# Optimization experiments

Hardware: AMD Instinct MI355X
Metric: run time of the kernel (lower is better)

Reference implementation:

```python
import jax, jax.numpy as jnp
import numpy as np

BINS = 70
HLO, HHI = -10.0, 10.0
EPS = 1e-5


def _conv_bn(x, w, b, g, be, relu=True):
    # 1x1 Conv1d == channel matmul: x [B,C,N], w [O,C]
    y = jnp.einsum('oc,bcn->bon', w, x) + b[None, :, None]
    # BatchNorm1d in training mode: biased batch stats over (batch, points)
    m = jnp.mean(y, axis=(0, 2))
    v = jnp.var(y, axis=(0, 2))
    y = (y - m[None, :, None]) * jax.lax.rsqrt(v + EPS)[None, :, None]
    y = y * g[None, :, None] + be[None, :, None]
    return jax.nn.relu(y) if relu else y


def _batch_hist(x):
    # Faithful to the torch.histc global-offset hack: one flat histogram with
    # bins*B*F buckets and group offsets of exactly (HHI-HLO); values that fall
    # outside [HLO,HHI] for a given (b,f) leak into neighboring groups, exactly
    # as in the original. Returns argmax bin index per (b,f) as float.
    B, F, N = x.shape
    w = (HHI - HLO) / BINS  # 2/7, and group offset 20 == BINS*w so bins align
    total = BINS * B * F
    grp = jnp.arange(B * F, dtype=jnp.int32).reshape(B, F, 1)
    gidx = jnp.floor((x - HLO) / w).astype(jnp.int32) + BINS * grp
    gidx = jnp.where((gidx >= 0) & (gidx < total), gidx, total)  # drop out-of-range
    counts = jnp.zeros(total + 1, jnp.float32).at[gidx.ravel()].add(1.0)
    h = counts[:total].reshape(B, F, BINS)
    return jnp.argmax(h, axis=-1).astype(jnp.float32)  # [B,F]


def setup_inputs() -> dict:
    key = jax.random.key(0)
    ks = jax.random.split(key, 7)
    d = {
        'x': jax.random.normal(ks[0], (16, 3, 4096), dtype=jnp.float32),
        'w1': jax.random.normal(ks[1], (64, 3), dtype=jnp.float32) * 0.2,
        'b1': jnp.zeros((64,), jnp.float32),
        'g1': jnp.ones((64,), jnp.float32),
        'be1': jnp.zeros((64,), jnp.float32),
        'w2': jax.random.normal(ks[2], (128, 64), dtype=jnp.float32) * 0.1,
        'b2': jnp.zeros((128,), jnp.float32),
        'g2': jnp.ones((128,), jnp.float32),
        'be2': jnp.zeros((128,), jnp.float32),
        'w3': jax.random.normal(ks[3], (1024, 128), dtype=jnp.float32) * 0.08,
        'b3': jnp.zeros((1024,), jnp.float32),
        'g3': jnp.ones((1024,), jnp.float32),
        'be3': jnp.zeros((1024,), jnp.float32),
    }
    return d


def reference(x, w1, b1, g1, be1, w2, b2, g2, be2, w3, b3, g3, be3):
    # PointNetEncoder forward, global_feat=True, robust_type='HS',
    # input/feature transforms disabled (trans, trans_feat are None).
    h = _conv_bn(x, w1, b1, g1, be1, relu=True)    # [B,64,N]
    h = _conv_bn(h, w2, b2, g2, be2, relu=True)    # [B,128,N]
    h = _conv_bn(h, w3, b3, g3, be3, relu=False)   # [B,1024,N]
    feat = _batch_hist(h)                          # [B,1024] mode-bin indices
    return feat
```

## Files before the change

### kernel.cpp

```cpp
#include <hip/hip_runtime.h>

#define EPSF 1e-5f
#define TOTBINS 1146880

typedef _Float16 v8h __attribute__((ext_vector_type(8)));
typedef _Float16 v4h __attribute__((ext_vector_type(4)));
typedef float v4f __attribute__((ext_vector_type(4)));

#define OFF_PARTX   1146880
#define OFF_W1F     1149952
#define OFF_B1F     1150144
#define OFF_PMU1    1150208
#define OFF_M1N     1166592
#define OFF_MU1     1170688
#define OFF_W2H     1170752
#define OFF_W2L     1174848
#define OFF_B2F     1178944
#define OFF_PMU2    1179072
#define OFF_M2N     1211840
#define OFF_MU2     1228224
#define OFF_W3H     1228352
#define OFF_W3L     1293888
#define OFF_B3F     1359424
#define OFF_H1H     1360448
#define OFF_H1L     3457600
#define OFF_H2H     5554752
#define OFF_H2L     9749056

#define GLL(src,dst) __builtin_amdgcn_global_load_lds( \
    (const __attribute__((address_space(1))) void*)(src), \
    (__attribute__((address_space(3))) void*)(dst), 16, 0, 0)

__global__ void k_statsX(const float* __restrict__ x, float* __restrict__ part){
  __shared__ float red[12][256];
  int t = threadIdx.x;
  int s = blockIdx.x*256 + t;
  int b = s >> 12, n = s & 4095;
  const float* xb = x + (size_t)b*12288 + n;
  float x0 = xb[0], x1 = xb[4096], x2 = xb[8192];
  float v[12] = {x0,x1,x2, x0*x0,x0*x1,x0*x2, x1*x1,x1*x2,x2*x2, 0.f,0.f,0.f};
  #pragma unroll
  for(int j=0;j<12;j++) red[j][t]=v[j];
  __syncthreads();
  for(int off=128; off>0; off>>=1){
    if(t<off){
      #pragma unroll
      for(int j=0;j<12;j++) red[j][t]+=red[j][t+off];
    }
    __syncthreads();
  }
  if(t<12) part[blockIdx.x*12+t]=red[t][0];
}

__global__ void k_fold1(const float* __restrict__ part,
                        const float* __restrict__ w1, const float* __restrict__ b1,
                        const float* __restrict__ g1, const float* __restrict__ be1,
                        float* __restrict__ W1f, float* __restrict__ B1f){
  __shared__ double S[12];
  int t=threadIdx.x;
  if(t<12){
    double a=0.0;
    for(int s=0;s<256;s++) a+=(double)part[s*12+t];
    S[t]=a;
  }
  __syncthreads();
  if(t<64){
    double inv = 1.0/65536.0;
    double mu[3]={S[0]*inv,S[1]*inv,S[2]*inv};
    double M[3][3];
    M[0][0]=S[3]*inv; M[0][1]=S[4]*inv; M[0][2]=S[5]*inv;
    M[1][1]=S[6]*inv; M[1][2]=S[7]*inv; M[2][2]=S[8]*inv;
    M[1][0]=M[0][1]; M[2][0]=M[0][2]; M[2][1]=M[1][2];
    double w[3]={(double)w1[t*3],(double)w1[t*3+1],(double)w1[t*3+2]};
    double wm=0.0, q=0.0;
    for(int c=0;c<3;c++){
      wm += w[c]*mu[c];
      for(int d=0;d<3;d++) q += w[c]*w[d]*M[c][d];
    }
    double var = q - wm*wm;
    double m = wm + (double)b1[t];
    double sc = (double)g1[t] / sqrt(var + (double)EPSF);
    for(int c=0;c<3;c++) W1f[t*3+c]=(float)(w[c]*sc);
    B1f[t]=(float)(((double)b1[t]-m)*sc + (double)be1[t]);
  }
}

__global__ void k_l1s1(const float* __restrict__ x, const float* __restrict__ W1f,
                       const float* __restrict__ B1f,
                       _Float16* __restrict__ h1h, _Float16* __restrict__ h1l,
                       float* __restrict__ partM, float* __restrict__ partMu){
  __shared__ __align__(16) float tl[64][68];
  __shared__ float Wls[192];
  __shared__ float Bls[64];
  int t=threadIdx.x, wg=blockIdx.x;
  int s0=wg*256;
  int b=s0>>12, n0=s0&4095;
  int ti=t&15, tj=t>>4;
  if(t<192) Wls[t]=W1f[t];
  if(t<64)  Bls[t]=B1f[t];
  float acc[4][4];
  #pragma unroll
  for(int i=0;i<4;i++){
    #pragma unroll
    for(int j=0;j<4;j++) acc[i][j]=0.f;
  }
  float mu=0.f;
  for(int tile=0; tile<4; tile++){
    int nb=n0+tile*64;
    __syncthreads();
    {
      int nr=t>>2, cq=(t&3)<<4;
      int n=nb+nr;
      const float* xb = x + (size_t)b*12288 + n;
      float x0=xb[0], x1=xb[4096], x2=xb[8192];
      size_t off = ((size_t)((b<<12)+n))<<6;
      #pragma unroll
      for(int q=0;q<2;q++){
        v8h vh, vl;
        float4 r0, r1;
        #pragma unroll
        for(int e=0;e<8;e++){
          int f=cq+q*8+e;
          float v = fmaf(Wls[f*3+2],x2, fmaf(Wls[f*3+1],x1, fmaf(Wls[f*3],x0, Bls[f])));
          v = v>0.f ? v : 0.f;
          _Float16 hh=(_Float16)v;
          _Float16 ll=(_Float16)(v-(float)hh);
          vh[e]=hh; vl[e]=ll;
          float rec=(float)hh+(float)ll;
          if(e<4) ((float*)&r0)[e]=rec; else ((float*)&r1)[e-4]=rec;
        }
        *(v8h*)(h1h+off+cq+q*8)=vh;
        *(v8h*)(h1l+off+cq+q*8)=vl;
        *(float4*)&tl[nr][cq+q*8]   = r0;
        *(float4*)&tl[nr][cq+q*8+4] = r1;
      }
    }
    __syncthreads();
    for(int k=0;k<64;k++){
      float4 av = *(const float4*)&tl[k][ti*4];
      float4 bv = *(const float4*)&tl[k][tj*4];
      float a[4]={av.x,av.y,av.z,av.w};
      float bb[4]={bv.x,bv.y,bv.z,bv.w};
      #pragma unroll
      for(int i=0;i<4;i++){
        #pragma unroll
        for(int j=0;j<4;j++) acc[i][j]=fmaf(a[i],bb[j],acc[i][j]);
      }
    }
    if(t<64){
      float ss=0.f;
      for(int k=0;k<64;k++) ss+=tl[k][t];
      mu+=ss;
    }
  }
  #pragma unroll
  for(int i=0;i<4;i++){
    #pragma unroll
    for(int j=0;j<4;j++)
      partM[(size_t)wg*4096+(ti*4+i)*64+(tj*4+j)]=acc[i][j];
  }
  if(t<64) partMu[wg*64+t]=mu;
}

__global__ void k_reduceM1(const float* __restrict__ partM, const float* __restrict__ partMu,
                           float* __restrict__ M1n, float* __restrict__ mu1){
  int e=blockIdx.x*256+threadIdx.x;
  double a=0.0;
  for(int s=0;s<256;s++) a+=(double)partM[(size_t)s*4096+e];
  M1n[e]=(float)(a/65536.0);
  if(e<64){
    double m=0.0;
    for(int s=0;s<256;s++) m+=(double)partMu[s*64+e];
    mu1[e]=(float)(m/65536.0);
  }
}

__global__ void k_fold2(const float* __restrict__ w2, const float* __restrict__ b2,
                        const float* __restrict__ g2, const float* __restrict__ be2,
                        const float* __restrict__ M1n, const float* __restrict__ mu1,
                        _Float16* __restrict__ w2h, _Float16* __restrict__ w2l,
                        float* __restrict__ B2f){
  int f=blockIdx.x, t=threadIdx.x;
  __shared__ float w[64];
  w[t]=w2[f*64+t];
  __syncthreads();
  double tm=0.0;
  for(int c=0;c<64;c++) tm += (double)w[c]*(double)M1n[c*64+t];
  double pv=tm*(double)w[t];
  double pm=(double)w[t]*(double)mu1[t];
  #pragma unroll
  for(int off=32;off>0;off>>=1){
    pv+=__shfl_xor(pv,off,64);
    pm+=__shfl_xor(pm,off,64);
  }
  double var=pv-pm*pm;
  double m=pm+(double)b2[f];
  double sc=(double)g2[f]/sqrt(var+(double)EPSF);
  float Wf=(float)((double)w[t]*sc);
  _Float16 hh=(_Float16)Wf;
  w2h[f*64+t]=hh;
  w2l[f*64+t]=(_Float16)(Wf-(float)hh);
  if(t==0) B2f[f]=(float)(((double)b2[f]-m)*sc+(double)be2[f]);
}

__global__ __launch_bounds__(256,4) void k_layer2(
    const _Float16* __restrict__ h1h, const _Float16* __restrict__ h1l,
    const _Float16* __restrict__ w2h, const _Float16* __restrict__ w2l,
    const float* __restrict__ B2f,
    _Float16* __restrict__ h2h, _Float16* __restrict__ h2l){
  __shared__ __align__(16) _Float16 stage[4][512];
  int t=threadIdx.x, wg=blockIdx.x;
  int wv=t>>6, l=t&63;
  int lrow=l&15, lgrp=l>>4;
  int b=wg>>6;
  int n0=(wg&63)<<6;
  v8h Ah[2][2], Al[2][2];
  #pragma unroll
  for(int T=0;T<2;T++){
    const _Float16* ph = w2h + (size_t)(wv*32 + T*16 + lrow)*64 + lgrp*8;
    const _Float16* pl = w2l + (size_t)(wv*32 + T*16 + lrow)*64 + lgrp*8;
    #pragma unroll
    for(int s=0;s<2;s++){
      Ah[T][s]=*(const v8h*)(ph+s*32);
      Al[T][s]=*(const v8h*)(pl+s*32);
    }
  }
  float bias[2][4];
  #pragma unroll
  for(int T=0;T<2;T++){
    #pragma unroll
    for(int rr=0;rr<4;rr++) bias[T][rr]=B2f[wv*32+T*16+lgrp*4+rr];
  }
  int ks=wv>>1, pln=wv&1;
  const _Float16* src = (pln ? h1l : h1h)
      + (((size_t)((b<<12)+n0+lrow))<<6) + ks*32 + lgrp*8;
  _Float16* dst = &stage[wv][0];
  for(int it=0; it<4; it++){
    GLL(src,dst);
    src += 1024;
    __syncthreads();
    v8h Bh[2],Bl[2];
    #pragma unroll
    for(int s=0;s<2;s++){
      Bh[s]=*(const v8h*)&stage[s*2  ][l*8];
      Bl[s]=*(const v8h*)&stage[s*2+1][l*8];
    }
    int n=n0+it*16+lrow;
    #pragma unroll
    for(int T=0;T<2;T++){
      v4f acc={bias[T][0],bias[T][1],bias[T][2],bias[T][3]};
      #pragma unroll
      for(int s=0;s<2;s++){
        acc=__builtin_amdgcn_mfma_f32_16x16x32_f16(Ah[T][s],Bh[s],acc,0,0,0);
        acc=__builtin_amdgcn_mfma_f32_16x16x32_f16(Ah[T][s],Bl[s],acc,0,0,0);
        acc=__builtin_amdgcn_mfma_f32_16x16x32_f16(Al[T][s],Bh[s],acc,0,0,0);
      }
      size_t o=(((size_t)((b<<12)+n))<<7) + wv*32 + T*16 + lgrp*4;
      v4h sh, sl4;
      #pragma unroll
      for(int rr=0;rr<4;rr++){
        float v=acc[rr];
        v = v>0.f ? v : 0.f;
        _Float16 hh=(_Float16)v;
        sh[rr]=hh;
        sl4[rr]=(_Float16)(v-(float)hh);
      }
      *(v4h*)(h2h+o)=sh;
      *(v4h*)(h2l+o)=sl4;
    }
    __syncthreads();
  }
}

__global__ void k_stats2(const _Float16* __restrict__ h2h, const _Float16* __restrict__ h2l,
                         float* __restrict__ partM, float* __restrict__ partMu){
  __shared__ __align__(16) float tl[64][132];
  int t=threadIdx.x, wg=blockIdx.x;
  int s0=wg*256;
  int b=s0>>12, n0=s0&4095;
  int ti=t&15, tj=t>>4;
  float acc[8][8];
  #pragma unroll
  for(int i=0;i<8;i++){
    #pragma unroll
    for(int j=0;j<8;j++) acc[i][j]=0.f;
  }
  float mu=0.f;
  for(int tile=0; tile<4; tile++){
    int nb=n0+tile*64;
    __syncthreads();
    {
      int nr=t>>2, cq=(t&3)<<5;
      const _Float16* ph = h2h + ((size_t)((b<<12)+nb+nr))*128 + cq;
      const _Float16* pl = h2l + ((size_t)((b<<12)+nb+nr))*128 + cq;
      #pragma unroll
      for(int q=0;q<4;q++){
        v8h hh=*(const v8h*)(ph+q*8);
        v8h ll=*(const v8h*)(pl+q*8);
        float4 v0=make_float4((float)hh[0]+(float)ll[0],(float)hh[1]+(float)ll[1],
                              (float)hh[2]+(float)ll[2],(float)hh[3]+(float)ll[3]);
        float4 v1=make_float4((float)hh[4]+(float)ll[4],(float)hh[5]+(float)ll[5],
                              (float)hh[6]+(float)ll[6],(float)hh[7]+(float)ll[7]);
        *(float4*)&tl[nr][cq+q*8]   = v0;
        *(float4*)&tl[nr][cq+q*8+4] = v1;
      }
    }
    __syncthreads();
    for(int k=0;k<64;k++){
      float4 a0=*(const float4*)&tl[k][ti*8];
      float4 a1=*(const float4*)&tl[k][ti*8+4];
      float4 b0=*(const float4*)&tl[k][tj*8];
      float4 b1=*(const float4*)&tl[k][tj*8+4];
      float a[8]={a0.x,a0.y,a0.z,a0.w,a1.x,a1.y,a1.z,a1.w};
      float bb[8]={b0.x,b0.y,b0.z,b0.w,b1.x,b1.y,b1.z,b1.w};
      #pragma unroll
      for(int i=0;i<8;i++){
        #pragma unroll
        for(int j=0;j<8;j++) acc[i][j]=fmaf(a[i],bb[j],acc[i][j]);
      }
    }
    if(t<128){
      float s=0.f;
      for(int k=0;k<64;k++) s+=tl[k][t];
      mu+=s;
    }
  }
  #pragma unroll
  for(int i=0;i<8;i++){
    #pragma unroll
    for(int j=0;j<8;j++)
      partM[(size_t)wg*16384+(ti*8+i)*128+(tj*8+j)]=acc[i][j];
  }
  if(t<128) partMu[wg*128+t]=mu;
}

__global__ void k_reduceM2(const float* __restrict__ partM, const float* __restrict__ partMu,
                           float* __restrict__ M2n, float* __restrict__ mu2){
  int e=blockIdx.x*256+threadIdx.x;
  double a=0.0;
  for(int s=0;s<256;s++) a+=(double)partM[(size_t)s*16384+e];
  M2n[e]=(float)(a/65536.0);
  if(e<128){
    double m=0.0;
    for(int s=0;s<256;s++) m+=(double)partMu[s*128+e];
    mu2[e]=(float)(m/65536.0);
  }
}

__global__ void k_fold3(const float* __restrict__ w3, const float* __restrict__ b3,
                        const float* __restrict__ g3, const float* __restrict__ be3,
                        const float* __restrict__ M2n, const float* __restrict__ mu2,
                        _Float16* __restrict__ w3h, _Float16* __restrict__ w3l,
                        float* __restrict__ B3f){
  int f=blockIdx.x, t=threadIdx.x;
  __shared__ float w[128];
  __shared__ double rv[2], rm[2];
  w[t]=w3[f*128+t];
  __syncthreads();
  double tm=0.0;
  for(int c=0;c<128;c++) tm += (double)w[c]*(double)M2n[c*128+t];
  double pv=tm*(double)w[t];
  double pm=(double)w[t]*(double)mu2[t];
  #pragma unroll
  for(int off=32;off>0;off>>=1){
    pv+=__shfl_xor(pv,off,64);
    pm+=__shfl_xor(pm,off,64);
  }
  if((t&63)==0){ rv[t>>6]=pv; rm[t>>6]=pm; }
  __syncthreads();
  double pmt=rm[0]+rm[1];
  double var=(rv[0]+rv[1]) - pmt*pmt;
  double m=pmt + (double)b3[f];
  double sc=(double)g3[f]/sqrt(var+(double)EPSF);
  float Wf=(float)((double)w[t]*sc);
  _Float16 hh=(_Float16)Wf;
  w3h[f*128+t]=hh;
  w3l[f*128+t]=(_Float16)(Wf-(float)hh);
  if(t==0) B3f[f]=(float)(((double)b3[f]-m)*sc+(double)be3[f]);
}

__global__ __launch_bounds__(256,4) void k_gemm3_hist(
    const _Float16* __restrict__ h2h, const _Float16* __restrict__ h2l,
    const _Float16* __restrict__ w3h, const _Float16* __restrict__ w3l,
    const float* __restrict__ B3f, unsigned int* __restrict__ hist){
  __shared__ __align__(16) _Float16 stage[2][8][512];
  __shared__ unsigned int lh[4480];
  int t=threadIdx.x, wg=blockIdx.x;
  int wv=t>>6, l=t&63;
  int lrow=l&15, lgrp=l>>4;
  int b=wg>>6;
  int r=wg&63;
  int f0=(r>>3)<<7;
  int sl=r&7;
  int base=70*((b<<10)+f0);
  for(int i=t;i<4480;i+=256) lh[i]=0u;

  v8h Ah[2][4], Al[2][4];
  #pragma unroll
  for(int T=0;T<2;T++){
    const _Float16* ph = w3h + (size_t)(f0 + wv*32 + T*16 + lrow)*128 + lgrp*8;
    const _Float16* pl = w3l + (size_t)(f0 + wv*32 + T*16 + lrow)*128 + lgrp*8;
    #pragma unroll
    for(int s=0;s<4;s++){
      Ah[T][s]=*(const v8h*)(ph+s*32);
      Al[T][s]=*(const v8h*)(pl+s*32);
    }
  }
  float biasL[2]; int base70L[2];
  #pragma unroll
  for(int T=0;T<2;T++){
    int fl_=wv*32+T*16+lrow;
    biasL[T]=B3f[f0+fl_];
    base70L[T]=fl_*70;
  }
  const float wbin=(10.0f-(-10.0f))/70.0f;
  const float inv_w=1.0f/wbin;
  const float off_w=10.0f*inv_w;

  const _Float16* pH = h2h + ((size_t)((b<<12)+sl*512+lrow))*128 + wv*32 + lgrp*8;
  const _Float16* pL = h2l + ((size_t)((b<<12)+sl*512+lrow))*128 + wv*32 + lgrp*8;

#define ISSUE(B_) { GLL(pH,&stage[B_][wv*2][0]); GLL(pL,&stage[B_][wv*2+1][0]); \
                    pH+=2048; pL+=2048; }
#define COMPUTE(B_) { \
    v4f acc0={biasL[0],biasL[0],biasL[0],biasL[0]}; \
    v4f acc1={biasL[1],biasL[1],biasL[1],biasL[1]}; \
    _Pragma("unroll") \
    for(int s=0;s<4;s++){ \
      v8h Bh=*(const v8h*)&stage[B_][s*2  ][l*8]; \
      v8h Bl=*(const v8h*)&stage[B_][s*2+1][l*8]; \
      acc0=__builtin_amdgcn_mfma_f32_16x16x32_f16(Bh,Ah[0][s],acc0,0,0,0); \
      acc0=__builtin_amdgcn_mfma_f32_16x16x32_f16(Bl,Ah[0][s],acc0,0,0,0); \
      acc0=__builtin_amdgcn_mfma_f32_16x16x32_f16(Bh,Al[0][s],acc0,0,0,0); \
      acc1=__builtin_amdgcn_mfma_f32_16x16x32_f16(Bh,Ah[1][s],acc1,0,0,0); \
      acc1=__builtin_amdgcn_mfma_f32_16x16x32_f16(Bl,Ah[1][s],acc1,0,0,0); \
      acc1=__builtin_amdgcn_mfma_f32_16x16x32_f16(Bh,Al[1][s],acc1,0,0,0); \
    } \
    _Pragma("unroll") \
    for(int T=0;T<2;T++){ \
      v4f accT = T ? acc1 : acc0; \
      _Pragma("unroll") \
      for(int rr=0;rr<4;rr++){ \
        float q=fmaf(accT[rr],inv_w,off_w); \
        int bin=(int)floorf(q); \
        int loc=base70L[T]+bin; \
        if((unsigned)loc<8960u){ \
          atomicAdd(&lh[loc>>1], 1u<<((loc&1)<<4)); \
        }else{ \
          int g=base+loc; \
          if(g>=0 && g<TOTBINS) atomicAdd(&hist[g],1u); \
        } \
      } \
    } }

  ISSUE(0);
  __syncthreads();
  for(int ii=0;ii<16;ii++){
    ISSUE(1);
    COMPUTE(0);
    __syncthreads();
    if(ii<15) ISSUE(0);
    COMPUTE(1);
    __syncthreads();
  }
#undef ISSUE
#undef COMPUTE
  for(int i=t;i<4480;i+=256){
    unsigned int c=lh[i];
    if(c&0xFFFFu) atomicAdd(&hist[base+2*i],   c&0xFFFFu);
    if(c>>16)     atomicAdd(&hist[base+2*i+1], c>>16);
  }
}

__global__ void k_argmax(const unsigned int* __restrict__ hist, float* __restrict__ out){
  int g = blockIdx.x*256 + threadIdx.x;
  const unsigned int* h = hist + (size_t)g*70;
  unsigned int best=h[0]; int arg=0;
  for(int k=1;k<70;k++){
    unsigned int c=h[k];
    if(c>best){ best=c; arg=k; }
  }
  out[g]=(float)arg;
}

extern "C" void kernel_launch(void* const* d_in, const int* in_sizes, int n_in,
                              void* d_out, int out_size, void* d_ws, size_t ws_size,
                              hipStream_t stream){
  const float* x  =(const float*)d_in[0];
  const float* w1 =(const float*)d_in[1];
  const float* b1 =(const float*)d_in[2];
  const float* g1 =(const float*)d_in[3];
  const float* be1=(const float*)d_in[4];
  const float* w2 =(const float*)d_in[5];
  const float* b2 =(const float*)d_in[6];
  const float* g2 =(const float*)d_in[7];
  const float* be2=(const float*)d_in[8];
  const float* w3 =(const float*)d_in[9];
  const float* b3 =(const float*)d_in[10];
  const float* g3 =(const float*)d_in[11];
  const float* be3=(const float*)d_in[12];

  float* ws=(float*)d_ws;
  unsigned int* hist=(unsigned int*)ws;
  float* partX = ws+OFF_PARTX;
  float* W1f   = ws+OFF_W1F;
  float* B1f   = ws+OFF_B1F;
  float* pMu1  = ws+OFF_PMU1;
  float* M1n   = ws+OFF_M1N;
  float* mu1   = ws+OFF_MU1;
  _Float16* w2h=(_Float16*)(ws+OFF_W2H);
  _Float16* w2l=(_Float16*)(ws+OFF_W2L);
  float* B2f   = ws+OFF_B2F;
  float* pMu2  = ws+OFF_PMU2;
  float* M2n   = ws+OFF_M2N;
  float* mu2   = ws+OFF_MU2;
  _Float16* w3h=(_Float16*)(ws+OFF_W3H);
  _Float16* w3l=(_Float16*)(ws+OFF_W3L);
  float* B3f   = ws+OFF_B3F;
  _Float16* h1h=(_Float16*)(ws+OFF_H1H);
  _Float16* h1l=(_Float16*)(ws+OFF_H1L);
  _Float16* h2h=(_Float16*)(ws+OFF_H2H);
  _Float16* h2l=(_Float16*)(ws+OFF_H2L);
  float* partM1=(float*)(ws+OFF_H2H);
  float* partM2=(float*)(ws+OFF_H1H);

  hipMemsetAsync(hist, 0, (size_t)TOTBINS*sizeof(unsigned int), stream);

  k_statsX  <<<256,256,0,stream>>>(x, partX);
  k_fold1   <<<1,  256,0,stream>>>(partX,w1,b1,g1,be1,W1f,B1f);
  k_l1s1    <<<256,256,0,stream>>>(x,W1f,B1f,h1h,h1l,partM1,pMu1);
  k_reduceM1<<<16, 256,0,stream>>>(partM1,pMu1,M1n,mu1);
  k_fold2   <<<128, 64,0,stream>>>(w2,b2,g2,be2,M1n,mu1,w2h,w2l,B2f);
  k_layer2  <<<1024,256,0,stream>>>(h1h,h1l,w2h,w2l,B2f,h2h,h2l);
  k_stats2  <<<256,256,0,stream>>>(h2h,h2l,partM2,pMu2);
  k_reduceM2<<<64, 256,0,stream>>>(partM2,pMu2,M2n,mu2);
  k_fold3   <<<1024,128,0,stream>>>(w3,b3,g3,be3,M2n,mu2,w3h,w3l,B3f);
  k_gemm3_hist<<<1024,256,0,stream>>>(h2h,h2l,w3h,w3l,B3f,hist);
  k_argmax  <<<64, 256,0,stream>>>(hist,(float*)d_out);
}
```

Measured before the change: 214.2 us.

## Double-buffer layer2 staging loads and split stats2 Gram work across two blocks

Result: faster. 203.3 us (median of 2 runs) (-5.1%).

```diff
diff --git a/kernel.cpp b/kernel.cpp
--- a/kernel.cpp
+++ b/kernel.cpp
@@ -208,12 +208,12 @@
     const _Float16* __restrict__ w2h, const _Float16* __restrict__ w2l,
     const float* __restrict__ B2f,
     _Float16* __restrict__ h2h, _Float16* __restrict__ h2l){
-  __shared__ __align__(16) _Float16 stage[4][512];
+  __shared__ __align__(16) _Float16 stage[2][4][512];
   int t=threadIdx.x, wg=blockIdx.x;
   int wv=t>>6, l=t&63;
   int lrow=l&15, lgrp=l>>4;
-  int b=wg>>6;
-  int n0=(wg&63)<<6;
+  int b=wg>>5;
+  int n0=(wg&31)<<7;
   v8h Ah[2][2], Al[2][2];
   #pragma unroll
   for(int T=0;T<2;T++){
@@ -234,54 +234,64 @@
   int ks=wv>>1, pln=wv&1;
   const _Float16* src = (pln ? h1l : h1h)
       + (((size_t)((b<<12)+n0+lrow))<<6) + ks*32 + lgrp*8;
-  _Float16* dst = &stage[wv][0];
-  for(int it=0; it<4; it++){
-    GLL(src,dst);
-    src += 1024;
-    __syncthreads();
-    v8h Bh[2],Bl[2];
-    #pragma unroll
-    for(int s=0;s<2;s++){
-      Bh[s]=*(const v8h*)&stage[s*2  ][l*8];
-      Bl[s]=*(const v8h*)&stage[s*2+1][l*8];
-    }
-    int n=n0+it*16+lrow;
-    #pragma unroll
-    for(int T=0;T<2;T++){
-      v4f acc={bias[T][0],bias[T][1],bias[T][2],bias[T][3]};
-      #pragma unroll
-      for(int s=0;s<2;s++){
-        acc=__builtin_amdgcn_mfma_f32_16x16x32_f16(Ah[T][s],Bh[s],acc,0,0,0);
-        acc=__builtin_amdgcn_mfma_f32_16x16x32_f16(Ah[T][s],Bl[s],acc,0,0,0);
-        acc=__builtin_amdgcn_mfma_f32_16x16x32_f16(Al[T][s],Bh[s],acc,0,0,0);
-      }
-      size_t o=(((size_t)((b<<12)+n))<<7) + wv*32 + T*16 + lgrp*4;
-      v4h sh, sl4;
-      #pragma unroll
-      for(int rr=0;rr<4;rr++){
-        float v=acc[rr];
-        v = v>0.f ? v : 0.f;
-        _Float16 hh=(_Float16)v;
-        sh[rr]=hh;
-        sl4[rr]=(_Float16)(v-(float)hh);
-      }
-      *(v4h*)(h2h+o)=sh;
-      *(v4h*)(h2l+o)=sl4;
-    }
-    __syncthreads();
-  }
+
+#define L2ISSUE(B_) { GLL(src,&stage[B_][wv][0]); src += 1024; }
+#define L2COMPUTE(B_,IT) { \
+    v8h Bh[2],Bl[2]; \
+    _Pragma("unroll") \
+    for(int s=0;s<2;s++){ \
+      Bh[s]=*(const v8h*)&stage[B_][s*2  ][l*8]; \
+      Bl[s]=*(const v8h*)&stage[B_][s*2+1][l*8]; \
+    } \
+    int n=n0+(IT)*16+lrow; \
+    _Pragma("unroll") \
+    for(int T=0;T<2;T++){ \
+      v4f acc={bias[T][0],bias[T][1],bias[T][2],bias[T][3]}; \
+      _Pragma("unroll") \
+      for(int s=0;s<2;s++){ \
+        acc=__builtin_amdgcn_mfma_f32_16x16x32_f16(Ah[T][s],Bh[s],acc,0,0,0); \
+        acc=__builtin_amdgcn_mfma_f32_16x16x32_f16(Ah[T][s],Bl[s],acc,0,0,0); \
+        acc=__builtin_amdgcn_mfma_f32_16x16x32_f16(Al[T][s],Bh[s],acc,0,0,0); \
+      } \
+      size_t o=(((size_t)((b<<12)+n))<<7) + wv*32 + T*16 + lgrp*4; \
+      v4h sh, sl4; \
+      _Pragma("unroll") \
+      for(int rr=0;rr<4;rr++){ \
+        float v=acc[rr]; \
+        v = v>0.f ? v : 0.f; \
+        _Float16 hh=(_Float16)v; \
+        sh[rr]=hh; \
+        sl4[rr]=(_Float16)(v-(float)hh); \
+      } \
+      *(v4h*)(h2h+o)=sh; \
+      *(v4h*)(h2l+o)=sl4; \
+    } }
+
+  L2ISSUE(0);
+  __syncthreads();
+  for(int ii=0;ii<4;ii++){
+    L2ISSUE(1);
+    L2COMPUTE(0,2*ii);
+    __syncthreads();
+    if(ii<3) L2ISSUE(0);
+    L2COMPUTE(1,2*ii+1);
+    __syncthreads();
+  }
+#undef L2ISSUE
+#undef L2COMPUTE
 }
 
 __global__ void k_stats2(const _Float16* __restrict__ h2h, const _Float16* __restrict__ h2l,
                          float* __restrict__ partM, float* __restrict__ partMu){
   __shared__ __align__(16) float tl[64][132];
   int t=threadIdx.x, wg=blockIdx.x;
-  int s0=wg*256;
+  int chunk=wg>>1, half=wg&1;
+  int s0=chunk*256;
   int b=s0>>12, n0=s0&4095;
   int ti=t&15, tj=t>>4;
-  float acc[8][8];
-  #pragma unroll
-  for(int i=0;i<8;i++){
+  float acc[4][8];
+  #pragma unroll
+  for(int i=0;i<4;i++){
     #pragma unroll
     for(int j=0;j<8;j++) acc[i][j]=0.f;
   }
@@ -307,31 +317,30 @@
     }
     __syncthreads();
     for(int k=0;k<64;k++){
-      float4 a0=*(const float4*)&tl[k][ti*8];
-      float4 a1=*(const float4*)&tl[k][ti*8+4];
+      float4 av=*(const float4*)&tl[k][half*64+ti*4];
       float4 b0=*(const float4*)&tl[k][tj*8];
       float4 b1=*(const float4*)&tl[k][tj*8+4];
-      float a[8]={a0.x,a0.y,a0.z,a0.w,a1.x,a1.y,a1.z,a1.w};
+      float a[4]={av.x,av.y,av.z,av.w};
       float bb[8]={b0.x,b0.y,b0.z,b0.w,b1.x,b1.y,b1.z,b1.w};
       #pragma unroll
-      for(int i=0;i<8;i++){
+      for(int i=0;i<4;i++){
         #pragma unroll
         for(int j=0;j<8;j++) acc[i][j]=fmaf(a[i],bb[j],acc[i][j]);
       }
     }
-    if(t<128){
+    if(t<64){
       float s=0.f;
-      for(int k=0;k<64;k++) s+=tl[k][t];
+      for(int k=0;k<64;k++) s+=tl[k][half*64+t];
       mu+=s;
     }
   }
   #pragma unroll
-  for(int i=0;i<8;i++){
+  for(int i=0;i<4;i++){
     #pragma unroll
     for(int j=0;j<8;j++)
-      partM[(size_t)wg*16384+(ti*8+i)*128+(tj*8+j)]=acc[i][j];
-  }
-  if(t<128) partMu[wg*128+t]=mu;
+      partM[(size_t)chunk*16384+(half*64+ti*4+i)*128+(tj*8+j)]=acc[i][j];
+  }
+  if(t<64) partMu[chunk*128+half*64+t]=mu;
 }
 
 __global__ void k_reduceM2(const float* __restrict__ partM, const float* __restrict__ partMu,
@@ -531,8 +540,8 @@
   k_l1s1    <<<256,256,0,stream>>>(x,W1f,B1f,h1h,h1l,partM1,pMu1);
   k_reduceM1<<<16, 256,0,stream>>>(partM1,pMu1,M1n,mu1);
   k_fold2   <<<128, 64,0,stream>>>(w2,b2,g2,be2,M1n,mu1,w2h,w2l,B2f);
-  k_layer2  <<<1024,256,0,stream>>>(h1h,h1l,w2h,w2l,B2f,h2h,h2l);
-  k_stats2  <<<256,256,0,stream>>>(h2h,h2l,partM2,pMu2);
+  k_layer2  <<<512,256,0,stream>>>(h1h,h1l,w2h,w2l,B2f,h2h,h2l);
+  k_stats2  <<<512,256,0,stream>>>(h2h,h2l,partM2,pMu2);
   k_reduceM2<<<64, 256,0,stream>>>(partM2,pMu2,M2n,mu2);
   k_fold3   <<<1024,128,0,stream>>>(w3,b3,g3,be3,M2n,mu2,w3h,w3l,B3f);
   k_gemm3_hist<<<1024,256,0,stream>>>(h2h,h2l,w3h,w3l,B3f,hist);
```
